# Kernel optimization log

Hardware: AMD Instinct MI355X
Metric: run time of the kernel (lower is better)

The kernel has to match this reference:

```python
import jax, jax.numpy as jnp
import numpy as np

NUM_TRAIN = 256  # num_train_anchors
N, A, T = 8, 131072, 64


def _make_boxes(key, shape2):
    # shape2 = (..., 2) of (y, x); returns valid boxes (y1, x1, y2, x2) in [0, 1]
    k1, k2 = jax.random.split(key)
    c1 = jax.random.uniform(k1, shape2, dtype=jnp.float32)
    c2 = jax.random.uniform(k2, shape2, dtype=jnp.float32)
    lo = jnp.minimum(c1, c2)
    hi = jnp.maximum(c1, c2)
    return jnp.stack([lo[..., 0], lo[..., 1], hi[..., 0], hi[..., 1]], axis=-1)


def setup_inputs() -> dict:
    key = jax.random.key(0)
    ka, kt, kp, kn = jax.random.split(key, 4)
    return {
        "anchors": _make_boxes(ka, (N, A, 2)),
        "true_bboxes": _make_boxes(kt, (N, T, 2)),
        "rand_pos": jax.random.uniform(kp, (N, A), dtype=jnp.float32),
        "rand_neg": jax.random.uniform(kn, (N, A), dtype=jnp.float32),
    }


def _bbox_overlap(anchors, gt):
    # anchors [A,4], gt [T,4] -> IoU [A,T]
    ay1, ax1, ay2, ax2 = [anchors[:, i] for i in range(4)]
    gy1, gx1, gy2, gx2 = [gt[:, i] for i in range(4)]
    a_area = (ay2 - ay1) * (ax2 - ax1)                       # [A]
    g_area = (gy2 - gy1) * (gx2 - gx1)                       # [T]
    ih = jnp.clip(jnp.minimum(ay2[:, None], gy2[None, :]) - jnp.maximum(ay1[:, None], gy1[None, :]), 0.0)
    iw = jnp.clip(jnp.minimum(ax2[:, None], gx2[None, :]) - jnp.maximum(ax1[:, None], gx1[None, :]), 0.0)
    inter = ih * iw                                          # [A,T]
    union = a_area[:, None] + g_area[None, :] - inter
    return jnp.where(union > 0, inter / jnp.where(union > 0, union, 1.0), 0.0)


def _rank_of(scores):
    # rank[i] = position of element i in ascending sort of scores
    order = jnp.argsort(scores)
    return jnp.zeros(scores.shape[0], jnp.int32).at[order].set(jnp.arange(scores.shape[0], dtype=jnp.int32))


def _compute_bbox_deltas(anchors, gt):
    # standard (dy, dx, dh, dw) encoding with safe denominators
    ah = anchors[:, 2] - anchors[:, 0]
    aw = anchors[:, 3] - anchors[:, 1]
    acy = anchors[:, 0] + 0.5 * ah
    acx = anchors[:, 1] + 0.5 * aw
    gh = gt[:, 2] - gt[:, 0]
    gw = gt[:, 3] - gt[:, 1]
    gcy = gt[:, 0] + 0.5 * gh
    gcx = gt[:, 1] + 0.5 * gw
    ah_s = jnp.where(ah > 0, ah, 1.0)
    aw_s = jnp.where(aw > 0, aw, 1.0)
    gh_s = jnp.where(gh > 0, gh, 1.0)
    gw_s = jnp.where(gw > 0, gw, 1.0)
    return jnp.stack([(gcy - acy) / ah_s, (gcx - acx) / aw_s,
                      jnp.log(gh_s / ah_s), jnp.log(gw_s / aw_s)], axis=-1)


def _get_targets(anchors, gt, r_pos, r_neg):
    na = anchors.shape[0]
    # strip_out_of_bounds_anchors: zero out anchors falling outside [0,1]^2 (keeps static shape)
    inb = (anchors[:, 0] >= 0) & (anchors[:, 1] >= 0) & (anchors[:, 2] <= 1) & (anchors[:, 3] <= 1)
    anchors = jnp.where(inb[:, None], anchors, 0.0)

    overlaps = _bbox_overlap(anchors, gt)                    # [A,T]

    # --- class assignment ---
    iou_max_val = jnp.max(overlaps, axis=1)                  # [A]
    classes = jnp.full((na,), -1, jnp.int32)
    classes = jnp.where(iou_max_val < 0.3, 0, classes)
    iou_max_anchor = jnp.argmax(overlaps, axis=0)            # [T] best anchor per gt
    pos_anchor = jnp.zeros((na,), jnp.int32).at[iou_max_anchor].set(1)
    classes = jnp.where(pos_anchor > 0, 1, classes)
    classes = jnp.where(iou_max_val >= 0.7, 1, classes)

    # --- subsample positives to NUM_TRAIN//2 (uniform random subset) ---
    pos = classes > 0
    rank_p = _rank_of(jnp.where(pos, r_pos, jnp.inf))
    keep_pos = pos & (rank_p < NUM_TRAIN // 2)
    classes = jnp.where(pos & ~keep_pos, -1, classes)
    n_pos = jnp.sum(keep_pos.astype(jnp.int32))

    # --- subsample negatives to NUM_TRAIN - n_pos ---
    desired_neg = NUM_TRAIN - n_pos
    neg = classes == 0
    rank_n = _rank_of(jnp.where(neg, r_neg, jnp.inf))
    keep_neg = neg & (rank_n < desired_neg)
    classes = jnp.where(neg & ~keep_neg, -1, classes)

    # --- deltas for positive anchors ---
    best_gt = jnp.argmax(overlaps, axis=1)                   # [A]
    deltas = _compute_bbox_deltas(anchors, gt[best_gt])      # [A,4]
    deltas = jnp.where((classes > 0)[:, None], deltas, 0.0)
    return classes, deltas


def reference(anchors, true_bboxes, rand_pos, rand_neg):
    classes, deltas = jax.vmap(_get_targets)(anchors, true_bboxes, rand_pos, rand_neg)
    return classes, deltas
```

## Files before the change

kernel.cpp:

```cpp
#include <hip/hip_runtime.h>
#include <stdint.h>

#define N_B 8
#define A_N 131072
#define T_N 64
#define NUM_TRAIN 256
#define NEG_TAU 0.05f
#define ITEM_CAP 512
#define HSET 512
#define APT 2
#define SEG_A 512
#define GBLK_A 256
#define CAPP 128

typedef unsigned long long u64;
typedef unsigned int u32;

__device__ __forceinline__ u64 aload64(const u64* p) {
    return __hip_atomic_load((u64*)p, __ATOMIC_RELAXED, __HIP_MEMORY_SCOPE_AGENT);
}
__device__ __forceinline__ int aload32(const int* p) {
    return __hip_atomic_load((int*)p, __ATOMIC_RELAXED, __HIP_MEMORY_SCOPE_AGENT);
}
__device__ __forceinline__ void astore64(u64* p, u64 v) {
    __hip_atomic_store(p, v, __ATOMIC_RELAXED, __HIP_MEMORY_SCOPE_AGENT);
}
__device__ __forceinline__ void astore32(int* p, int v) {
    __hip_atomic_store(p, v, __ATOMIC_RELAXED, __HIP_MEMORY_SCOPE_AGENT);
}

__device__ __forceinline__ float iou_one(float ay1, float ax1, float ay2, float ax2,
                                         float a_area, float gy1, float gx1, float gy2,
                                         float gx2, float g_area) {
#pragma clang fp contract(off)
    float ih = fmaxf(fminf(ay2, gy2) - fmaxf(ay1, gy1), 0.0f);
    float iw = fmaxf(fminf(ax2, gx2) - fmaxf(ax1, gx1), 0.0f);
    float inter = ih * iw;
    float uni = (a_area + g_area) - inter;
    return uni > 0.0f ? inter / uni : 0.0f;
}

__device__ __forceinline__ bool in_hset(const int* hset, int a) {
    u32 h = ((u32)a * 2654435761u) >> 23 & (HSET - 1);
    while (true) {
        int v = hset[h];
        if (v == -1) return false;
        if (v == a) return true;
        h = (h + 1) & (HSET - 1);
    }
}

__device__ u64 tail_select(const u64* list, const int* cnts,
                           const u64* extras, int ecnt, const int* hset, bool use_excl,
                           int k, float scale, u64 ovf_all,
                           int* hist, u64* items, int* misc, int* wsum, u64* result) {
    int tid = threadIdx.x, lane = tid & 63, wid = tid >> 6;
    if (tid == 0) { misc[0] = 0; *result = ovf_all; }
    __syncthreads();

    int h = hist[tid], v = h;
#pragma unroll
    for (int d = 1; d < 64; d <<= 1) {
        int t = __shfl_up(v, d, 64);
        if (lane >= d) v += t;
    }
    if (lane == 63) wsum[wid] = v;
    __syncthreads();
    int total = wsum[0] + wsum[1] + wsum[2] + wsum[3];
    int base = 0;
    for (int w = 0; w < wid; w++) base += wsum[w];
    int incl = base + v, exc = incl - h;
    if (k >= exc && k < incl) { misc[1] = tid; misc[2] = exc; }
    if (tid == 0) misc[3] = total;
    __syncthreads();
    if (k >= total) return ovf_all;
    int b = misc[1], before = misc[2];

#define PROC(P) do { u64 p_ = (P); int a_ = (int)(u32)p_;                                   \
        if (!use_excl || !in_hset(hset, a_)) {                                              \
            float v_ = __uint_as_float((u32)(p_ >> 32));                                    \
            int bn_ = (int)(v_ * scale); bn_ = bn_ > 255 ? 255 : bn_;                       \
            if (bn_ == b) { int ix_ = atomicAdd(&misc[0], 1);                               \
                            if (ix_ < ITEM_CAP) items[ix_] = p_; } } } while (0)

    int c = aload32(&cnts[tid]);
    const u64* lp = list + ((size_t)tid << 7);
    for (int ci = 0; ci < c; ci += 4) {
        u64 p0 = aload64(&lp[ci]);
        u64 p1 = (ci + 1 < c) ? aload64(&lp[ci + 1]) : 0;
        u64 p2 = (ci + 2 < c) ? aload64(&lp[ci + 2]) : 0;
        u64 p3 = (ci + 3 < c) ? aload64(&lp[ci + 3]) : 0;
        PROC(p0);
        if (ci + 1 < c) PROC(p1);
        if (ci + 2 < c) PROC(p2);
        if (ci + 3 < c) PROC(p3);
    }
    for (int i = tid; i < ecnt; i += 256) PROC(extras[i]);
#undef PROC
    __syncthreads();
    int m = misc[0]; m = m < ITEM_CAP ? m : ITEM_CAP;
    int target = k - before;
    for (int i = tid; i < m; i += 256) {
        u64 p = items[i];
        int r = 0;
        for (int j = 0; j < m; j++) r += (items[j] < p);
        if (r == target) *result = p;
    }
    __syncthreads();
    u64 res = *result;
    __syncthreads();
    return res;
}

__global__ void __launch_bounds__(256, 8) k_fused(const float4* __restrict__ anchors4,
                                                  const float4* __restrict__ gts4,
                                                  const float* __restrict__ rpos,
                                                  const float* __restrict__ rneg,
                                                  long long* __restrict__ colpack,
                                                  u64* __restrict__ pos_list,
                                                  u64* __restrict__ neg_list,
                                                  int* __restrict__ bcp, int* __restrict__ bcn,
                                                  int* __restrict__ hist_pos,
                                                  int* __restrict__ hist_neg,
                                                  int* __restrict__ done_cnt,
                                                  u64* __restrict__ cutoff,
                                                  float* __restrict__ out_classes,
                                                  float4* __restrict__ out_deltas) {
    __shared__ float4 gbox[T_N];
    __shared__ float gars[T_N];
    __shared__ u64 cmax[T_N];
    __shared__ int lcnt[2];
    __shared__ signed char c0s[SEG_A];
    __shared__ u32 wbm[16];
    __shared__ int hist[256];
    __shared__ u64 items[ITEM_CAP];
    __shared__ int hset[HSET];
    __shared__ u64 extras[T_N];
    __shared__ int wnrs[T_N];
    __shared__ int misc[4];
    __shared__ int wsum[4];
    __shared__ int shr[4];
    __shared__ u64 result;
    __shared__ u64 scut[2];
    __shared__ int slast;

    int n = blockIdx.y, bx = blockIdx.x, tid = threadIdx.x, lane = tid & 63;
    int a0 = bx * SEG_A + tid;
    size_t nA = (size_t)n * A_N;

    if (tid < T_N) {
        float4 gb = gts4[n * T_N + tid];
        gbox[tid] = gb;
        {
#pragma clang fp contract(off)
            gars[tid] = (gb.z - gb.x) * (gb.w - gb.y);
        }
        cmax[tid] = 0;
    }
    if (tid < 2) lcnt[tid] = 0;
    if (tid < 16) wbm[tid] = 0;
    __syncthreads();

    float ay1[APT], ax1[APT], ay2[APT], ax2[APT], aar[APT], vmax[APT];
#pragma unroll
    for (int k = 0; k < APT; k++) {
        float4 ab = anchors4[nA + a0 + k * 256];
        float y1 = ab.x, x1 = ab.y, y2 = ab.z, x2 = ab.w;
        bool inb = (y1 >= 0.f) && (x1 >= 0.f) && (y2 <= 1.f) && (x2 <= 1.f);
        if (!inb) { y1 = x1 = y2 = x2 = 0.f; }
        ay1[k] = y1; ax1[k] = x1; ay2[k] = y2; ax2[k] = x2;
        {
#pragma clang fp contract(off)
            aar[k] = (y2 - y1) * (x2 - x1);
        }
        vmax[k] = 0.f;
    }

#pragma unroll 4
    for (int jj = 0; jj < T_N; jj++) {
        int j = (lane + jj) & (T_N - 1);
        float4 gb = gbox[j];
        float gar = gars[j];
        float vb = iou_one(ay1[0], ax1[0], ay2[0], ax2[0], aar[0], gb.x, gb.y, gb.z, gb.w, gar);
        vmax[0] = fmaxf(vmax[0], vb);
        int kb = 0;
#pragma unroll
        for (int k = 1; k < APT; k++) {
            float v = iou_one(ay1[k], ax1[k], ay2[k], ax2[k], aar[k], gb.x, gb.y, gb.z, gb.w, gar);
            vmax[k] = fmaxf(vmax[k], v);
            if (v > vb) { vb = v; kb = k; }
        }
        u64 pk = ((u64)__float_as_uint(vb) << 32) | (u32)(~(u32)(a0 + (kb << 8)));
        atomicMax(&cmax[j], pk);
    }

    int myc0[APT];
    float myrp[APT], myrn[APT];
    size_t segbase = ((size_t)(n * GBLK_A + bx)) << 7;
#pragma unroll
    for (int k = 0; k < APT; k++) {
        int a = a0 + k * 256;
        float vm = vmax[k];
        int c0 = (vm < 0.3f) ? 0 : ((vm >= 0.7f) ? 1 : -1);
        myc0[k] = c0;
        c0s[tid + k * 256] = (signed char)c0;
        float rp = rpos[nA + a], rn = rneg[nA + a];
        myrp[k] = rp; myrn[k] = rn;
        if (c0 == 1) {
            int sl = atomicAdd(&lcnt[0], 1);
            if (sl < CAPP) {
                astore64(&pos_list[segbase + sl], ((u64)__float_as_uint(rp) << 32) | (u32)a);
                int bb = (int)(rp * 256.0f); bb = bb > 255 ? 255 : bb;
                atomicAdd(&hist_pos[(n << 8) + bb], 1);
            }
        } else if (c0 == 0) {
            if (rn < NEG_TAU) {
                int sl = atomicAdd(&lcnt[1], 1);
                if (sl < CAPP) {
                    astore64(&neg_list[segbase + sl], ((u64)__float_as_uint(rn) << 32) | (u32)a);
                    int bb = (int)(rn * (256.0f / NEG_TAU)); bb = bb > 255 ? 255 : bb;
                    atomicAdd(&hist_neg[(n << 8) + bb], 1);
                }
            }
        }
    }
    __syncthreads();

    if (tid < T_N) {
        u64 m = cmax[tid];
        u32 wg = ~(u32)m;
        int wl = (int)wg - bx * SEG_A;
        u32 enc = (u32)c0s[wl] & 3u;
        u64 pk = (m & 0xFFFFFFFF00000000ull) | (u32)(~((wg << 2) | enc));
        atomicMax(&colpack[(n << 6) + tid], (long long)pk);
    }
    if (tid == 0) {
        astore32(&bcp[n * GBLK_A + bx], lcnt[0] < CAPP ? lcnt[0] : CAPP);
        astore32(&bcn[n * GBLK_A + bx], lcnt[1] < CAPP ? lcnt[1] : CAPP);
    }

    asm volatile("s_waitcnt vmcnt(0) lgkmcnt(0)" ::: "memory");
    __syncthreads();
    if (tid == 0) slast = (atomicAdd(&done_cnt[n], 1) == GBLK_A - 1) ? 1 : 0;
    __syncthreads();

    if (slast) {
        for (int i = tid; i < HSET; i += 256) hset[i] = -1;
        hist[tid] = aload32(&hist_pos[(n << 8) + tid]);
        __syncthreads();

        int w = 0, pcv = 0;
        bool dup = false;
        if (tid < T_N) {
            u64 m = aload64((const u64*)&colpack[(n << 6) + tid]);
            u32 ie = ~(u32)m;
            w = (int)(ie >> 2);
            pcv = ((ie & 3u) == 3u) ? -1 : (int)(ie & 3u);
            wnrs[tid] = w;
            u32 hh = ((u32)w * 2654435761u) >> 23 & (HSET - 1);
            while (true) {
                int old = atomicCAS(&hset[hh], -1, w);
                if (old == -1 || old == w) break;
                hh = (hh + 1) & (HSET - 1);
            }
        }
        __syncthreads();
        if (tid < T_N) {
            for (int t2 = 0; t2 < tid; t2++) dup |= (wnrs[t2] == w);
            bool val = !dup && (pcv != 1);
            u64 mask = __ballot(val);
            if (val) {
                int ix = (int)__popcll(mask & ((1ull << tid) - 1));
                extras[ix] = ((u64)__float_as_uint(rpos[nA + w]) << 32) | (u32)w;
            }
            if (tid == 0) shr[0] = (int)__popcll(mask);
        }
        __syncthreads();
        int extra_cnt = shr[0];
        for (int i = tid; i < extra_cnt; i += 256) {
            float vv = __uint_as_float((u32)(extras[i] >> 32));
            int bb = (int)(vv * 256.0f); bb = bb > 255 ? 255 : bb;
            atomicAdd(&hist[bb], 1);
        }
        __syncthreads();

        u64 cp = tail_select(pos_list + (((size_t)n * GBLK_A) << 7), bcp + n * GBLK_A,
                             extras, extra_cnt, hset, false,
                             NUM_TRAIN / 2, 256.0f, ~0ull,
                             hist, items, misc, wsum, &result);
        int P = misc[3];

        hist[tid] = aload32(&hist_neg[(n << 8) + tid]);
        __syncthreads();
        if (tid < T_N && !dup && pcv == 0) {
            float r = rneg[nA + w];
            if (r < NEG_TAU) {
                int bb = (int)(r * (256.0f / NEG_TAU)); bb = bb > 255 ? 255 : bb;
                atomicAdd(&hist[bb], -1);
            }
        }
        __syncthreads();
        int n_pos = P < NUM_TRAIN / 2 ? P : NUM_TRAIN / 2;
        u64 cn = tail_select(neg_list + (((size_t)n * GBLK_A) << 7), bcn + n * GBLK_A,
                             nullptr, 0, hset, true,
                             NUM_TRAIN - n_pos, 256.0f / NEG_TAU,
                             ((u64)__float_as_uint(NEG_TAU) << 32),
                             hist, items, misc, wsum, &result);
        if (tid == 0) {
            astore64(&cutoff[2 * n], cp);
            astore64(&cutoff[2 * n + 1], cn);
            scut[0] = cp; scut[1] = cn;
        }
    } else if (tid == 0) {
        u64 v;
        do { v = aload64(&cutoff[2 * n]); if (v != 0) break; __builtin_amdgcn_s_sleep(8); } while (true);
        scut[0] = v;
        do { v = aload64(&cutoff[2 * n + 1]); if (v != 0) break; __builtin_amdgcn_s_sleep(2); } while (true);
        scut[1] = v;
    }
    __syncthreads();
    u64 cp = scut[0], cn = scut[1];

    if (tid < T_N) {
        u64 m = aload64((const u64*)&colpack[(n << 6) + tid]);
        int w = (int)((~(u32)m) >> 2);
        int d = w - bx * SEG_A;
        if ((u32)d < (u32)SEG_A) atomicOr(&wbm[d >> 5], 1u << (d & 31));
    }
    __syncthreads();

#pragma unroll
    for (int k = 0; k < APT; k++) {
        int l = tid + k * 256;
        int a = a0 + k * 256;
        int c = myc0[k];
        if ((wbm[l >> 5] >> (l & 31)) & 1) c = 1;
        int fc = -1;
        if (c == 1) {
            u64 p = ((u64)__float_as_uint(myrp[k]) << 32) | (u32)a;
            fc = (p < cp) ? 1 : -1;
        } else if (c == 0) {
            u64 p = ((u64)__float_as_uint(myrn[k]) << 32) | (u32)a;
            fc = (p < cn) ? 0 : -1;
        }
        out_classes[nA + a] = (float)fc;

        float4 d = make_float4(0.f, 0.f, 0.f, 0.f);
        if (fc == 1) {
            float vm = 0.f; int jb = 0;
            for (int t = 0; t < T_N; t++) {
                float4 gb = gbox[t];
                float v = iou_one(ay1[k], ax1[k], ay2[k], ax2[k], aar[k],
                                  gb.x, gb.y, gb.z, gb.w, gars[t]);
                bool g = v > vm;
                vm = g ? v : vm;
                jb = g ? t : jb;
            }
            float4 gb = gbox[jb];
            float ah = ay2[k] - ay1[k], aw = ax2[k] - ax1[k];
            float acy = ay1[k] + 0.5f * ah, acx = ax1[k] + 0.5f * aw;
            float gh = gb.z - gb.x, gw = gb.w - gb.y;
            float gcy = gb.x + 0.5f * gh, gcx = gb.y + 0.5f * gw;
            float ah_s = ah > 0.f ? ah : 1.f, aw_s = aw > 0.f ? aw : 1.f;
            float gh_s = gh > 0.f ? gh : 1.f, gw_s = gw > 0.f ? gw : 1.f;
            d.x = (gcy - acy) / ah_s;
            d.y = (gcx - acx) / aw_s;
            d.z = logf(gh_s / ah_s);
            d.w = logf(gw_s / aw_s);
        }
        out_deltas[nA + a] = d;
    }
}

extern "C" void kernel_launch(void* const* d_in, const int* in_sizes, int n_in,
                              void* d_out, int out_size, void* d_ws, size_t ws_size,
                              hipStream_t stream) {
    const float4* anchors4 = (const float4*)d_in[0];
    const float4* gts4     = (const float4*)d_in[1];
    const float*  rpos     = (const float*)d_in[2];
    const float*  rneg     = (const float*)d_in[3];

    char* p = (char*)d_ws;
    u64* cutoff     = (u64*)p; p += 2 * N_B * sizeof(u64);
    int* hist_pos_g = (int*)p; p += N_B * 256 * sizeof(int);
    int* hist_neg_g = (int*)p; p += N_B * 256 * sizeof(int);
    int* done_cnt   = (int*)p; p += N_B * sizeof(int);
    long long* colpack = (long long*)p; p += N_B * T_N * sizeof(long long);
    u64* pos_list = (u64*)p;  p += (size_t)N_B * GBLK_A * CAPP * sizeof(u64);
    u64* neg_list = (u64*)p;  p += (size_t)N_B * GBLK_A * CAPP * sizeof(u64);
    int* bcp  = (int*)p;  p += N_B * GBLK_A * sizeof(int);
    int* bcn  = (int*)p;  p += N_B * GBLK_A * sizeof(int);

    float* out_classes = (float*)d_out;
    float4* out_deltas = (float4*)((float*)d_out + (size_t)N_B * A_N);

    size_t zbytes = 2 * N_B * sizeof(u64) + (2 * N_B * 256 + N_B) * sizeof(int);
    hipMemsetAsync(cutoff, 0, zbytes, stream);

    k_fused<<<dim3(GBLK_A, N_B), 256, 0, stream>>>(anchors4, gts4, rpos, rneg,
                                                   colpack, pos_list, neg_list, bcp, bcn,
                                                   hist_pos_g, hist_neg_g, done_cnt, cutoff,
                                                   out_classes, out_deltas);
}
```

Baseline: 184.1 us.

## Split fused kernel into selection kernel and vectorized output kernel, removing spin-wait

The single fused kernel had every block spin-wait on a global cutoff that the last-finishing block computed, then write outputs. Now the first kernel stores a byte pre-class per anchor and only the last block computes the cutoffs. A second kernel reads the pre-classes, random values and cutoffs with vector loads and writes classes as float4. It recomputes IoU and deltas only for the few positive anchors. This removes the grid-wide busy wait and the dependence on co-residency, at the cost of an extra launch and a round trip of the pre-class bytes through global memory.

```diff
diff --git a/kernel.cpp b/kernel.cpp
--- a/kernel.cpp
+++ b/kernel.cpp
@@ -12,6 +12,8 @@
 #define SEG_A 512
 #define GBLK_A 256
 #define CAPP 128
+#define BLK_C 128
+#define SEG_C 1024
 
 typedef unsigned long long u64;
 typedef unsigned int u32;
@@ -112,26 +114,24 @@
     return res;
 }
 
-__global__ void __launch_bounds__(256, 8) k_fused(const float4* __restrict__ anchors4,
-                                                  const float4* __restrict__ gts4,
-                                                  const float* __restrict__ rpos,
-                                                  const float* __restrict__ rneg,
-                                                  long long* __restrict__ colpack,
-                                                  u64* __restrict__ pos_list,
-                                                  u64* __restrict__ neg_list,
-                                                  int* __restrict__ bcp, int* __restrict__ bcn,
-                                                  int* __restrict__ hist_pos,
-                                                  int* __restrict__ hist_neg,
-                                                  int* __restrict__ done_cnt,
-                                                  u64* __restrict__ cutoff,
-                                                  float* __restrict__ out_classes,
-                                                  float4* __restrict__ out_deltas) {
+__global__ void __launch_bounds__(256) k_main(const float4* __restrict__ anchors4,
+                                              const float4* __restrict__ gts4,
+                                              const float* __restrict__ rpos,
+                                              const float* __restrict__ rneg,
+                                              unsigned char* __restrict__ preclass,
+                                              long long* __restrict__ colpack,
+                                              u64* __restrict__ pos_list,
+                                              u64* __restrict__ neg_list,
+                                              int* __restrict__ bcp, int* __restrict__ bcn,
+                                              int* __restrict__ hist_pos,
+                                              int* __restrict__ hist_neg,
+                                              int* __restrict__ done_cnt,
+                                              u64* __restrict__ cutoff) {
     __shared__ float4 gbox[T_N];
     __shared__ float gars[T_N];
     __shared__ u64 cmax[T_N];
     __shared__ int lcnt[2];
     __shared__ signed char c0s[SEG_A];
-    __shared__ u32 wbm[16];
     __shared__ int hist[256];
     __shared__ u64 items[ITEM_CAP];
     __shared__ int hset[HSET];
@@ -141,7 +141,6 @@
     __shared__ int wsum[4];
     __shared__ int shr[4];
     __shared__ u64 result;
-    __shared__ u64 scut[2];
     __shared__ int slast;
 
     int n = blockIdx.y, bx = blockIdx.x, tid = threadIdx.x, lane = tid & 63;
@@ -158,7 +157,6 @@
         cmax[tid] = 0;
     }
     if (tid < 2) lcnt[tid] = 0;
-    if (tid < 16) wbm[tid] = 0;
     __syncthreads();
 
     float ay1[APT], ax1[APT], ay2[APT], ax2[APT], aar[APT], vmax[APT];
@@ -194,19 +192,16 @@
         atomicMax(&cmax[j], pk);
     }
 
-    int myc0[APT];
-    float myrp[APT], myrn[APT];
     size_t segbase = ((size_t)(n * GBLK_A + bx)) << 7;
 #pragma unroll
     for (int k = 0; k < APT; k++) {
         int a = a0 + k * 256;
         float vm = vmax[k];
         int c0 = (vm < 0.3f) ? 0 : ((vm >= 0.7f) ? 1 : -1);
-        myc0[k] = c0;
         c0s[tid + k * 256] = (signed char)c0;
-        float rp = rpos[nA + a], rn = rneg[nA + a];
-        myrp[k] = rp; myrn[k] = rn;
+        preclass[nA + a] = (unsigned char)(signed char)c0;
         if (c0 == 1) {
+            float rp = rpos[nA + a];
             int sl = atomicAdd(&lcnt[0], 1);
             if (sl < CAPP) {
                 astore64(&pos_list[segbase + sl], ((u64)__float_as_uint(rp) << 32) | (u32)a);
@@ -214,6 +209,7 @@
                 atomicAdd(&hist_pos[(n << 8) + bb], 1);
             }
         } else if (c0 == 0) {
+            float rn = rneg[nA + a];
             if (rn < NEG_TAU) {
                 int sl = atomicAdd(&lcnt[1], 1);
                 if (sl < CAPP) {
@@ -243,122 +239,166 @@
     __syncthreads();
     if (tid == 0) slast = (atomicAdd(&done_cnt[n], 1) == GBLK_A - 1) ? 1 : 0;
     __syncthreads();
-
-    if (slast) {
-        for (int i = tid; i < HSET; i += 256) hset[i] = -1;
-        hist[tid] = aload32(&hist_pos[(n << 8) + tid]);
-        __syncthreads();
-
-        int w = 0, pcv = 0;
-        bool dup = false;
-        if (tid < T_N) {
-            u64 m = aload64((const u64*)&colpack[(n << 6) + tid]);
-            u32 ie = ~(u32)m;
-            w = (int)(ie >> 2);
-            pcv = ((ie & 3u) == 3u) ? -1 : (int)(ie & 3u);
-            wnrs[tid] = w;
-            u32 hh = ((u32)w * 2654435761u) >> 23 & (HSET - 1);
-            while (true) {
-                int old = atomicCAS(&hset[hh], -1, w);
-                if (old == -1 || old == w) break;
-                hh = (hh + 1) & (HSET - 1);
-            }
-        }
-        __syncthreads();
-        if (tid < T_N) {
-            for (int t2 = 0; t2 < tid; t2++) dup |= (wnrs[t2] == w);
-            bool val = !dup && (pcv != 1);
-            u64 mask = __ballot(val);
-            if (val) {
-                int ix = (int)__popcll(mask & ((1ull << tid) - 1));
-                extras[ix] = ((u64)__float_as_uint(rpos[nA + w]) << 32) | (u32)w;
-            }
-            if (tid == 0) shr[0] = (int)__popcll(mask);
-        }
-        __syncthreads();
-        int extra_cnt = shr[0];
-        for (int i = tid; i < extra_cnt; i += 256) {
-            float vv = __uint_as_float((u32)(extras[i] >> 32));
-            int bb = (int)(vv * 256.0f); bb = bb > 255 ? 255 : bb;
-            atomicAdd(&hist[bb], 1);
-        }
-        __syncthreads();
-
-        u64 cp = tail_select(pos_list + (((size_t)n * GBLK_A) << 7), bcp + n * GBLK_A,
-                             extras, extra_cnt, hset, false,
-                             NUM_TRAIN / 2, 256.0f, ~0ull,
-                             hist, items, misc, wsum, &result);
-        int P = misc[3];
-
-        hist[tid] = aload32(&hist_neg[(n << 8) + tid]);
-        __syncthreads();
-        if (tid < T_N && !dup && pcv == 0) {
-            float r = rneg[nA + w];
-            if (r < NEG_TAU) {
-                int bb = (int)(r * (256.0f / NEG_TAU)); bb = bb > 255 ? 255 : bb;
-                atomicAdd(&hist[bb], -1);
-            }
-        }
-        __syncthreads();
-        int n_pos = P < NUM_TRAIN / 2 ? P : NUM_TRAIN / 2;
-        u64 cn = tail_select(neg_list + (((size_t)n * GBLK_A) << 7), bcn + n * GBLK_A,
-                             nullptr, 0, hset, true,
-                             NUM_TRAIN - n_pos, 256.0f / NEG_TAU,
-                             ((u64)__float_as_uint(NEG_TAU) << 32),
-                             hist, items, misc, wsum, &result);
-        if (tid == 0) {
-            astore64(&cutoff[2 * n], cp);
-            astore64(&cutoff[2 * n + 1], cn);
-            scut[0] = cp; scut[1] = cn;
-        }
-    } else if (tid == 0) {
-        u64 v;
-        do { v = aload64(&cutoff[2 * n]); if (v != 0) break; __builtin_amdgcn_s_sleep(8); } while (true);
-        scut[0] = v;
-        do { v = aload64(&cutoff[2 * n + 1]); if (v != 0) break; __builtin_amdgcn_s_sleep(2); } while (true);
-        scut[1] = v;
-    }
-    __syncthreads();
-    u64 cp = scut[0], cn = scut[1];
-
+    if (!slast) return;
+
+    for (int i = tid; i < HSET; i += 256) hset[i] = -1;
+    hist[tid] = aload32(&hist_pos[(n << 8) + tid]);
+    __syncthreads();
+
+    int w = 0, pcv = 0;
+    bool dup = false;
     if (tid < T_N) {
         u64 m = aload64((const u64*)&colpack[(n << 6) + tid]);
-        int w = (int)((~(u32)m) >> 2);
-        int d = w - bx * SEG_A;
-        if ((u32)d < (u32)SEG_A) atomicOr(&wbm[d >> 5], 1u << (d & 31));
-    }
-    __syncthreads();
-
-#pragma unroll
-    for (int k = 0; k < APT; k++) {
-        int l = tid + k * 256;
-        int a = a0 + k * 256;
-        int c = myc0[k];
-        if ((wbm[l >> 5] >> (l & 31)) & 1) c = 1;
+        u32 ie = ~(u32)m;
+        w = (int)(ie >> 2);
+        pcv = ((ie & 3u) == 3u) ? -1 : (int)(ie & 3u);
+        wnrs[tid] = w;
+        u32 hh = ((u32)w * 2654435761u) >> 23 & (HSET - 1);
+        while (true) {
+            int old = atomicCAS(&hset[hh], -1, w);
+            if (old == -1 || old == w) break;
+            hh = (hh + 1) & (HSET - 1);
+        }
+    }
+    __syncthreads();
+    if (tid < T_N) {
+        for (int t2 = 0; t2 < tid; t2++) dup |= (wnrs[t2] == w);
+        bool val = !dup && (pcv != 1);
+        u64 mask = __ballot(val);
+        if (val) {
+            int ix = (int)__popcll(mask & ((1ull << tid) - 1));
+            extras[ix] = ((u64)__float_as_uint(rpos[nA + w]) << 32) | (u32)w;
+        }
+        if (tid == 0) shr[0] = (int)__popcll(mask);
+    }
+    __syncthreads();
+    int extra_cnt = shr[0];
+    for (int i = tid; i < extra_cnt; i += 256) {
+        float vv = __uint_as_float((u32)(extras[i] >> 32));
+        int bb = (int)(vv * 256.0f); bb = bb > 255 ? 255 : bb;
+        atomicAdd(&hist[bb], 1);
+    }
+    __syncthreads();
+
+    u64 cp = tail_select(pos_list + (((size_t)n * GBLK_A) << 7), bcp + n * GBLK_A,
+                         extras, extra_cnt, hset, false,
+                         NUM_TRAIN / 2, 256.0f, ~0ull,
+                         hist, items, misc, wsum, &result);
+    int P = misc[3];
+
+    hist[tid] = aload32(&hist_neg[(n << 8) + tid]);
+    __syncthreads();
+    if (tid < T_N && !dup && pcv == 0) {
+        float r = rneg[nA + w];
+        if (r < NEG_TAU) {
+            int bb = (int)(r * (256.0f / NEG_TAU)); bb = bb > 255 ? 255 : bb;
+            atomicAdd(&hist[bb], -1);
+        }
+    }
+    __syncthreads();
+    int n_pos = P < NUM_TRAIN / 2 ? P : NUM_TRAIN / 2;
+    u64 cn = tail_select(neg_list + (((size_t)n * GBLK_A) << 7), bcn + n * GBLK_A,
+                         nullptr, 0, hset, true,
+                         NUM_TRAIN - n_pos, 256.0f / NEG_TAU,
+                         ((u64)__float_as_uint(NEG_TAU) << 32),
+                         hist, items, misc, wsum, &result);
+    if (tid == 0) {
+        cutoff[2 * n] = cp;
+        cutoff[2 * n + 1] = cn;
+    }
+}
+
+__global__ void __launch_bounds__(256) k_C(const float4* __restrict__ anchors4,
+                                           const float4* __restrict__ gts4,
+                                           const u32* __restrict__ preclass32,
+                                           const long long* __restrict__ colpack,
+                                           const float4* __restrict__ rpos4,
+                                           const float4* __restrict__ rneg4,
+                                           const u64* __restrict__ cutoff,
+                                           float4* __restrict__ out_classes4,
+                                           float4* __restrict__ out_deltas) {
+    __shared__ float4 gbox[T_N];
+    __shared__ float gars[T_N];
+    __shared__ u32 wbm[32];
+    __shared__ u32 pbm[32];
+    int n = blockIdx.y, bx = blockIdx.x, tid = threadIdx.x;
+    size_t nA = (size_t)n * A_N;
+    if (tid < 32) { wbm[tid] = 0; pbm[tid] = 0; }
+    __syncthreads();
+    if (tid < T_N) {
+        float4 gb = gts4[n * T_N + tid];
+        gbox[tid] = gb;
+        {
+#pragma clang fp contract(off)
+            gars[tid] = (gb.z - gb.x) * (gb.w - gb.y);
+        }
+        int w = (int)((~(u32)(u64)colpack[(n << 6) + tid]) >> 2);
+        int d = w - bx * SEG_C;
+        if ((u32)d < (u32)SEG_C) atomicOr(&wbm[d >> 5], 1u << (d & 31));
+    }
+    __syncthreads();
+
+    size_t gi4 = nA / 4 + bx * 256 + tid;
+    u32 pcw = preclass32[gi4];
+    float4 rp = rpos4[gi4];
+    float4 rn = rneg4[gi4];
+    float rpv[4] = {rp.x, rp.y, rp.z, rp.w};
+    float rnv[4] = {rn.x, rn.y, rn.z, rn.w};
+    int a0 = (bx * 256 + tid) * 4;
+    u64 cp = cutoff[2 * n], cn = cutoff[2 * n + 1];
+
+    u32 marked = (wbm[tid >> 3] >> ((tid & 7) * 4)) & 0xF;
+
+    float fcv[4];
+#pragma unroll
+    for (int j = 0; j < 4; j++) {
+        int c = (int)(signed char)((pcw >> (8 * j)) & 0xFF);
+        if ((marked >> j) & 1) c = 1;
+        int a = a0 + j;
         int fc = -1;
         if (c == 1) {
-            u64 p = ((u64)__float_as_uint(myrp[k]) << 32) | (u32)a;
+            u64 p = ((u64)__float_as_uint(rpv[j]) << 32) | (u32)a;
             fc = (p < cp) ? 1 : -1;
         } else if (c == 0) {
-            u64 p = ((u64)__float_as_uint(myrn[k]) << 32) | (u32)a;
+            u64 p = ((u64)__float_as_uint(rnv[j]) << 32) | (u32)a;
             fc = (p < cn) ? 0 : -1;
         }
-        out_classes[nA + a] = (float)fc;
-
+        fcv[j] = (float)fc;
+        if (fc == 1) {
+            int s = 4 * tid + j;
+            atomicOr(&pbm[s >> 5], 1u << (s & 31));
+        }
+    }
+    out_classes4[gi4] = make_float4(fcv[0], fcv[1], fcv[2], fcv[3]);
+    __syncthreads();
+
+    int base = bx * SEG_C;
+#pragma unroll
+    for (int j = 0; j < 4; j++) {
+        int s = j * 256 + tid;
         float4 d = make_float4(0.f, 0.f, 0.f, 0.f);
-        if (fc == 1) {
+        if ((pbm[s >> 5] >> (s & 31)) & 1) {
+            int a = base + s;
+            float4 ab = anchors4[nA + a];
+            float ay1 = ab.x, ax1 = ab.y, ay2 = ab.z, ax2 = ab.w;
+            bool inb = (ay1 >= 0.f) && (ax1 >= 0.f) && (ay2 <= 1.f) && (ax2 <= 1.f);
+            if (!inb) { ay1 = ax1 = ay2 = ax2 = 0.f; }
+            float a_area;
+            {
+#pragma clang fp contract(off)
+                a_area = (ay2 - ay1) * (ax2 - ax1);
+            }
             float vm = 0.f; int jb = 0;
             for (int t = 0; t < T_N; t++) {
                 float4 gb = gbox[t];
-                float v = iou_one(ay1[k], ax1[k], ay2[k], ax2[k], aar[k],
-                                  gb.x, gb.y, gb.z, gb.w, gars[t]);
+                float v = iou_one(ay1, ax1, ay2, ax2, a_area, gb.x, gb.y, gb.z, gb.w, gars[t]);
                 bool g = v > vm;
                 vm = g ? v : vm;
                 jb = g ? t : jb;
             }
             float4 gb = gbox[jb];
-            float ah = ay2[k] - ay1[k], aw = ax2[k] - ax1[k];
-            float acy = ay1[k] + 0.5f * ah, acx = ax1[k] + 0.5f * aw;
+            float ah = ay2 - ay1, aw = ax2 - ax1;
+            float acy = ay1 + 0.5f * ah, acx = ax1 + 0.5f * aw;
             float gh = gb.z - gb.x, gw = gb.w - gb.y;
             float gcy = gb.x + 0.5f * gh, gcx = gb.y + 0.5f * gw;
             float ah_s = ah > 0.f ? ah : 1.f, aw_s = aw > 0.f ? aw : 1.f;
@@ -368,7 +408,7 @@
             d.z = logf(gh_s / ah_s);
             d.w = logf(gw_s / aw_s);
         }
-        out_deltas[nA + a] = d;
+        out_deltas[nA + base + s] = d;
     }
 }
 
@@ -381,24 +421,27 @@
     const float*  rneg     = (const float*)d_in[3];
 
     char* p = (char*)d_ws;
-    u64* cutoff     = (u64*)p; p += 2 * N_B * sizeof(u64);
     int* hist_pos_g = (int*)p; p += N_B * 256 * sizeof(int);
     int* hist_neg_g = (int*)p; p += N_B * 256 * sizeof(int);
     int* done_cnt   = (int*)p; p += N_B * sizeof(int);
+    u64* cutoff   = (u64*)p;  p += 2 * N_B * sizeof(u64);
     long long* colpack = (long long*)p; p += N_B * T_N * sizeof(long long);
     u64* pos_list = (u64*)p;  p += (size_t)N_B * GBLK_A * CAPP * sizeof(u64);
     u64* neg_list = (u64*)p;  p += (size_t)N_B * GBLK_A * CAPP * sizeof(u64);
+    unsigned char* preclass = (unsigned char*)p; p += (size_t)N_B * A_N;
     int* bcp  = (int*)p;  p += N_B * GBLK_A * sizeof(int);
     int* bcn  = (int*)p;  p += N_B * GBLK_A * sizeof(int);
 
-    float* out_classes = (float*)d_out;
-    float4* out_deltas = (float4*)((float*)d_out + (size_t)N_B * A_N);
-
-    size_t zbytes = 2 * N_B * sizeof(u64) + (2 * N_B * 256 + N_B) * sizeof(int);
-    hipMemsetAsync(cutoff, 0, zbytes, stream);
-
-    k_fused<<<dim3(GBLK_A, N_B), 256, 0, stream>>>(anchors4, gts4, rpos, rneg,
-                                                   colpack, pos_list, neg_list, bcp, bcn,
-                                                   hist_pos_g, hist_neg_g, done_cnt, cutoff,
-                                                   out_classes, out_deltas);
-}
+    float4* out_classes4 = (float4*)d_out;
+    float4* out_deltas   = (float4*)((float*)d_out + (size_t)N_B * A_N);
+
+    hipMemsetAsync(hist_pos_g, 0, (2 * N_B * 256 + N_B) * sizeof(int), stream);
+
+    k_main<<<dim3(GBLK_A, N_B), 256, 0, stream>>>(anchors4, gts4, rpos, rneg, preclass,
+                                                  colpack, pos_list, neg_list, bcp, bcn,
+                                                  hist_pos_g, hist_neg_g, done_cnt, cutoff);
+    k_C<<<dim3(BLK_C, N_B), 256, 0, stream>>>(anchors4, gts4, (const u32*)preclass,
+                                              colpack, (const float4*)rpos,
+                                              (const float4*)rneg, cutoff,
+                                              out_classes4, out_deltas);
+}
```

Measured after the change: 184.7 us. Within noise of the previous version (+0.4%).

## Bucket candidates by histogram bin so tail select scans only target bin

Applied to the files above, without the earlier changes.

Positive and negative candidates are now written straight into per-image, per-histogram-bin global buckets, using the global histogram atomic as the slot index. The last block's tail selection then reads only the one bin that holds the k-th element, instead of scanning every per-block list and filtering. The waiting blocks now poll a single ready flag with a longer sleep instead of polling the two cutoff values. This removes per-block shared counters and the long serial list scan, but adds global atomic contention on hot bins and caps each bin at 128 entries, so overflow in a dense bin could make the selection inexact.

```diff
diff --git a/kernel.cpp b/kernel.cpp
--- a/kernel.cpp
+++ b/kernel.cpp
@@ -6,12 +6,12 @@
 #define T_N 64
 #define NUM_TRAIN 256
 #define NEG_TAU 0.05f
-#define ITEM_CAP 512
+#define ITEM_CAP 256
 #define HSET 512
 #define APT 2
 #define SEG_A 512
 #define GBLK_A 256
-#define CAPP 128
+#define BINCAP 128
 
 typedef unsigned long long u64;
 typedef unsigned int u32;
@@ -50,7 +50,7 @@
     }
 }
 
-__device__ u64 tail_select(const u64* list, const int* cnts,
+__device__ u64 tail_select(const u64* bybin, const int* gcnt,
                            const u64* extras, int ecnt, const int* hset, bool use_excl,
                            int k, float scale, u64 ovf_all,
                            int* hist, u64* items, int* misc, int* wsum, u64* result) {
@@ -76,27 +76,21 @@
     if (k >= total) return ovf_all;
     int b = misc[1], before = misc[2];
 
-#define PROC(P) do { u64 p_ = (P); int a_ = (int)(u32)p_;                                   \
-        if (!use_excl || !in_hset(hset, a_)) {                                              \
-            float v_ = __uint_as_float((u32)(p_ >> 32));                                    \
-            int bn_ = (int)(v_ * scale); bn_ = bn_ > 255 ? 255 : bn_;                       \
-            if (bn_ == b) { int ix_ = atomicAdd(&misc[0], 1);                               \
-                            if (ix_ < ITEM_CAP) items[ix_] = p_; } } } while (0)
-
-    int c = aload32(&cnts[tid]);
-    const u64* lp = list + ((size_t)tid << 7);
-    for (int ci = 0; ci < c; ci += 4) {
-        u64 p0 = aload64(&lp[ci]);
-        u64 p1 = (ci + 1 < c) ? aload64(&lp[ci + 1]) : 0;
-        u64 p2 = (ci + 2 < c) ? aload64(&lp[ci + 2]) : 0;
-        u64 p3 = (ci + 3 < c) ? aload64(&lp[ci + 3]) : 0;
-        PROC(p0);
-        if (ci + 1 < c) PROC(p1);
-        if (ci + 2 < c) PROC(p2);
-        if (ci + 3 < c) PROC(p3);
-    }
-    for (int i = tid; i < ecnt; i += 256) PROC(extras[i]);
-#undef PROC
+    int stored = gcnt[b]; stored = stored > BINCAP ? BINCAP : stored;
+    for (int i = tid; i < stored; i += 256) {
+        u64 p = aload64(&bybin[(size_t)b * BINCAP + i]);
+        int a = (int)(u32)p;
+        if (!use_excl || !in_hset(hset, a)) {
+            int ix = atomicAdd(&misc[0], 1);
+            if (ix < ITEM_CAP) items[ix] = p;
+        }
+    }
+    for (int i = tid; i < ecnt; i += 256) {
+        u64 p = extras[i];
+        float vv = __uint_as_float((u32)(p >> 32));
+        int bn = (int)(vv * scale); bn = bn > 255 ? 255 : bn;
+        if (bn == b) { int ix = atomicAdd(&misc[0], 1); if (ix < ITEM_CAP) items[ix] = p; }
+    }
     __syncthreads();
     int m = misc[0]; m = m < ITEM_CAP ? m : ITEM_CAP;
     int target = k - before;
@@ -112,27 +106,27 @@
     return res;
 }
 
-__global__ void __launch_bounds__(256, 8) k_fused(const float4* __restrict__ anchors4,
-                                                  const float4* __restrict__ gts4,
-                                                  const float* __restrict__ rpos,
-                                                  const float* __restrict__ rneg,
-                                                  long long* __restrict__ colpack,
-                                                  u64* __restrict__ pos_list,
-                                                  u64* __restrict__ neg_list,
-                                                  int* __restrict__ bcp, int* __restrict__ bcn,
-                                                  int* __restrict__ hist_pos,
-                                                  int* __restrict__ hist_neg,
-                                                  int* __restrict__ done_cnt,
-                                                  u64* __restrict__ cutoff,
-                                                  float* __restrict__ out_classes,
-                                                  float4* __restrict__ out_deltas) {
+__global__ void __launch_bounds__(256) k_fused(const float4* __restrict__ anchors4,
+                                               const float4* __restrict__ gts4,
+                                               const float* __restrict__ rpos,
+                                               const float* __restrict__ rneg,
+                                               long long* __restrict__ colpack,
+                                               u64* __restrict__ pos_bybin,
+                                               u64* __restrict__ neg_bybin,
+                                               int* __restrict__ hist_pos,
+                                               int* __restrict__ hist_neg,
+                                               int* __restrict__ done_cnt,
+                                               int* __restrict__ flag,
+                                               u64* __restrict__ cutoff,
+                                               float* __restrict__ out_classes,
+                                               float4* __restrict__ out_deltas) {
     __shared__ float4 gbox[T_N];
     __shared__ float gars[T_N];
     __shared__ u64 cmax[T_N];
-    __shared__ int lcnt[2];
     __shared__ signed char c0s[SEG_A];
     __shared__ u32 wbm[16];
     __shared__ int hist[256];
+    __shared__ int gcnt[256];
     __shared__ u64 items[ITEM_CAP];
     __shared__ int hset[HSET];
     __shared__ u64 extras[T_N];
@@ -157,7 +151,6 @@
         }
         cmax[tid] = 0;
     }
-    if (tid < 2) lcnt[tid] = 0;
     if (tid < 16) wbm[tid] = 0;
     __syncthreads();
 
@@ -196,7 +189,6 @@
 
     int myc0[APT];
     float myrp[APT], myrn[APT];
-    size_t segbase = ((size_t)(n * GBLK_A + bx)) << 7;
 #pragma unroll
     for (int k = 0; k < APT; k++) {
         int a = a0 + k * 256;
@@ -207,20 +199,18 @@
         float rp = rpos[nA + a], rn = rneg[nA + a];
         myrp[k] = rp; myrn[k] = rn;
         if (c0 == 1) {
-            int sl = atomicAdd(&lcnt[0], 1);
-            if (sl < CAPP) {
-                astore64(&pos_list[segbase + sl], ((u64)__float_as_uint(rp) << 32) | (u32)a);
-                int bb = (int)(rp * 256.0f); bb = bb > 255 ? 255 : bb;
-                atomicAdd(&hist_pos[(n << 8) + bb], 1);
-            }
+            int bb = (int)(rp * 256.0f); bb = bb > 255 ? 255 : bb;
+            int sl = atomicAdd(&hist_pos[(n << 8) + bb], 1);
+            if (sl < BINCAP)
+                astore64(&pos_bybin[(size_t)((n << 8) + bb) * BINCAP + sl],
+                         ((u64)__float_as_uint(rp) << 32) | (u32)a);
         } else if (c0 == 0) {
             if (rn < NEG_TAU) {
-                int sl = atomicAdd(&lcnt[1], 1);
-                if (sl < CAPP) {
-                    astore64(&neg_list[segbase + sl], ((u64)__float_as_uint(rn) << 32) | (u32)a);
-                    int bb = (int)(rn * (256.0f / NEG_TAU)); bb = bb > 255 ? 255 : bb;
-                    atomicAdd(&hist_neg[(n << 8) + bb], 1);
-                }
+                int bb = (int)(rn * (256.0f / NEG_TAU)); bb = bb > 255 ? 255 : bb;
+                int sl = atomicAdd(&hist_neg[(n << 8) + bb], 1);
+                if (sl < BINCAP)
+                    astore64(&neg_bybin[(size_t)((n << 8) + bb) * BINCAP + sl],
+                             ((u64)__float_as_uint(rn) << 32) | (u32)a);
             }
         }
     }
@@ -234,10 +224,6 @@
         u64 pk = (m & 0xFFFFFFFF00000000ull) | (u32)(~((wg << 2) | enc));
         atomicMax(&colpack[(n << 6) + tid], (long long)pk);
     }
-    if (tid == 0) {
-        astore32(&bcp[n * GBLK_A + bx], lcnt[0] < CAPP ? lcnt[0] : CAPP);
-        astore32(&bcn[n * GBLK_A + bx], lcnt[1] < CAPP ? lcnt[1] : CAPP);
-    }
 
     asm volatile("s_waitcnt vmcnt(0) lgkmcnt(0)" ::: "memory");
     __syncthreads();
@@ -246,7 +232,11 @@
 
     if (slast) {
         for (int i = tid; i < HSET; i += 256) hset[i] = -1;
-        hist[tid] = aload32(&hist_pos[(n << 8) + tid]);
+        {
+            int gp = aload32(&hist_pos[(n << 8) + tid]);
+            gcnt[tid] = gp;
+            hist[tid] = gp;
+        }
         __syncthreads();
 
         int w = 0, pcv = 0;
@@ -284,13 +274,17 @@
         }
         __syncthreads();
 
-        u64 cp = tail_select(pos_list + (((size_t)n * GBLK_A) << 7), bcp + n * GBLK_A,
+        u64 cp = tail_select(pos_bybin + ((size_t)(n << 8)) * BINCAP, gcnt,
                              extras, extra_cnt, hset, false,
                              NUM_TRAIN / 2, 256.0f, ~0ull,
                              hist, items, misc, wsum, &result);
         int P = misc[3];
 
-        hist[tid] = aload32(&hist_neg[(n << 8) + tid]);
+        {
+            int g = aload32(&hist_neg[(n << 8) + tid]);
+            gcnt[tid] = g;
+            hist[tid] = g;
+        }
         __syncthreads();
         if (tid < T_N && !dup && pcv == 0) {
             float r = rneg[nA + w];
@@ -301,7 +295,7 @@
         }
         __syncthreads();
         int n_pos = P < NUM_TRAIN / 2 ? P : NUM_TRAIN / 2;
-        u64 cn = tail_select(neg_list + (((size_t)n * GBLK_A) << 7), bcn + n * GBLK_A,
+        u64 cn = tail_select(neg_bybin + ((size_t)(n << 8)) * BINCAP, gcnt,
                              nullptr, 0, hset, true,
                              NUM_TRAIN - n_pos, 256.0f / NEG_TAU,
                              ((u64)__float_as_uint(NEG_TAU) << 32),
@@ -309,14 +303,14 @@
         if (tid == 0) {
             astore64(&cutoff[2 * n], cp);
             astore64(&cutoff[2 * n + 1], cn);
+            asm volatile("s_waitcnt vmcnt(0)" ::: "memory");
+            astore32(&flag[n], 1);
             scut[0] = cp; scut[1] = cn;
         }
     } else if (tid == 0) {
-        u64 v;
-        do { v = aload64(&cutoff[2 * n]); if (v != 0) break; __builtin_amdgcn_s_sleep(8); } while (true);
-        scut[0] = v;
-        do { v = aload64(&cutoff[2 * n + 1]); if (v != 0) break; __builtin_amdgcn_s_sleep(2); } while (true);
-        scut[1] = v;
+        while (aload32(&flag[n]) == 0) __builtin_amdgcn_s_sleep(64);
+        scut[0] = aload64(&cutoff[2 * n]);
+        scut[1] = aload64(&cutoff[2 * n + 1]);
     }
     __syncthreads();
     u64 cp = scut[0], cn = scut[1];
@@ -381,24 +375,22 @@
     const float*  rneg     = (const float*)d_in[3];
 
     char* p = (char*)d_ws;
-    u64* cutoff     = (u64*)p; p += 2 * N_B * sizeof(u64);
     int* hist_pos_g = (int*)p; p += N_B * 256 * sizeof(int);
     int* hist_neg_g = (int*)p; p += N_B * 256 * sizeof(int);
     int* done_cnt   = (int*)p; p += N_B * sizeof(int);
+    int* flag       = (int*)p; p += N_B * sizeof(int);
+    u64* cutoff   = (u64*)p;  p += 2 * N_B * sizeof(u64);
     long long* colpack = (long long*)p; p += N_B * T_N * sizeof(long long);
-    u64* pos_list = (u64*)p;  p += (size_t)N_B * GBLK_A * CAPP * sizeof(u64);
-    u64* neg_list = (u64*)p;  p += (size_t)N_B * GBLK_A * CAPP * sizeof(u64);
-    int* bcp  = (int*)p;  p += N_B * GBLK_A * sizeof(int);
-    int* bcn  = (int*)p;  p += N_B * GBLK_A * sizeof(int);
+    u64* pos_bybin = (u64*)p; p += (size_t)N_B * 256 * BINCAP * sizeof(u64);
+    u64* neg_bybin = (u64*)p; p += (size_t)N_B * 256 * BINCAP * sizeof(u64);
 
     float* out_classes = (float*)d_out;
     float4* out_deltas = (float4*)((float*)d_out + (size_t)N_B * A_N);
 
-    size_t zbytes = 2 * N_B * sizeof(u64) + (2 * N_B * 256 + N_B) * sizeof(int);
-    hipMemsetAsync(cutoff, 0, zbytes, stream);
+    hipMemsetAsync(hist_pos_g, 0, (2 * N_B * 256 + 2 * N_B) * sizeof(int), stream);
 
     k_fused<<<dim3(GBLK_A, N_B), 256, 0, stream>>>(anchors4, gts4, rpos, rneg,
-                                                   colpack, pos_list, neg_list, bcp, bcn,
-                                                   hist_pos_g, hist_neg_g, done_cnt, cutoff,
-                                                   out_classes, out_deltas);
-}
+                                                   colpack, pos_bybin, neg_bybin,
+                                                   hist_pos_g, hist_neg_g, done_cnt, flag,
+                                                   cutoff, out_classes, out_deltas);
+}
```

After: 253.6 us. 37.8% more time.
